# Kernel optimization log

Measured on AMD Instinct MI355X. Metric: run time of the kernel, lower is better.

The kernel has to match this reference:

```python
import jax, jax.numpy as jnp
import numpy as np

D = 1024
H = 4
HD = D // H
B = 256
L = 64
DILATIONS = (1, 4, 8, 16)


def setup_inputs() -> dict:
    key = jax.random.key(0)
    ks = jax.random.split(key, 12)
    s = 1.0 / np.sqrt(D)
    return {
        "x": jax.random.normal(ks[0], (B, D), jnp.float32),
        "hist": jax.random.normal(ks[1], (L, B, D), jnp.float32),
        "Wq": jax.random.normal(ks[2], (D, D), jnp.float32) * s,
        "bq": jnp.zeros((D,), jnp.float32),
        "Wk": jax.random.normal(ks[3], (D, D), jnp.float32) * s,
        "bk": jnp.zeros((D,), jnp.float32),
        "Wv": jax.random.normal(ks[4], (D, D), jnp.float32) * s,
        "bv": jnp.zeros((D,), jnp.float32),
        "Wo": jax.random.normal(ks[5], (D, D), jnp.float32) * s,
        "bo": jnp.zeros((D,), jnp.float32),
        "dil_w": jnp.full((len(DILATIONS),), 1.0 / len(DILATIONS), jnp.float32),
        "gamma": jnp.ones((D,), jnp.float32),
        "beta": jnp.zeros((D,), jnp.float32),
    }


def reference(x, hist, Wq, bq, Wk, bk, Wv, bv, Wo, bo, dil_w, gamma, beta):
    scale = 1.0 / np.sqrt(HD)
    q = (x @ Wq + bq).reshape(B, H, HD)  # (B, H, HD)
    attended = []
    for d in DILATIONS:
        # history frames at stride d, concatenated along dim 0 (faithful to torch.cat)
        frames = hist[::d].reshape(-1, D)              # (T', D), T' = ceil(L/d)*B
        k = (frames @ Wk + bk).reshape(-1, H, HD)      # (T', H, HD)
        v = (frames @ Wv + bv).reshape(-1, H, HD)
        s = jnp.einsum('bhd,thd->bht', q, k) * scale   # (B, H, T')
        a = jax.nn.softmax(s, axis=-1)
        attended.append(jnp.einsum('bht,thd->bhd', a, v).reshape(B, D))
    w = jax.nn.softmax(dil_w, axis=0)
    combined = sum(w[i] * attended[i] for i in range(len(DILATIONS)))
    y = x + combined @ Wo + bo
    mu = jnp.mean(y, axis=-1, keepdims=True)
    var = jnp.var(y, axis=-1, keepdims=True)
    return (y - mu) / jnp.sqrt(var + 1e-5) * gamma + beta
```

## Files before the change

kernel.cpp:

```cpp
#include <hip/hip_runtime.h>


#define DD    1024
#define TALL  16384

typedef _Float16 half8  __attribute__((ext_vector_type(8)));
typedef _Float16 half4v __attribute__((ext_vector_type(4)));
typedef float    floatx4 __attribute__((ext_vector_type(4)));
typedef unsigned int u32;

static const size_t OFF_WOT  = 0;
static const size_t OFF_WV16 = 2097152;
static const size_t OFF_WK16 = 4194304;
static const size_t OFF_WQ16 = 6291456;
static const size_t OFF_XB   = 8388608;
static const size_t OFF_G    = 8912896;
static const size_t OFF_WVOT = 11010048;
static const size_t OFF_WQKT = 19398656;
static const size_t OFF_BVWO = 27787264;
static const size_t OFF_BQK  = 27791360;
static const size_t OFF_PHR  = 27807744;
static const size_t OFF_OPP  = 29904896;
static const size_t OFF_HB   = 38293504;
static const size_t OFF_HT   = 71848960;
static const size_t OFF_S    = 105403392;

__device__ __forceinline__ size_t chunk16_off(int g) {
  if (g < 4)  return (size_t)g * 2097152;
  if (g < 8)  return 19398656 + (size_t)(g - 4) * 2097152;
  if (g < 12) return 29904896 + (size_t)(g - 8) * 2097152;
  return 38293504 + (size_t)(g - 12) * 2097152;
}

__device__ __forceinline__ int frame_of(int g, int j) {
  if (g < 12) { int m = g * 4 + j; return m + m / 3 + 1; }
  if (g < 14) return 4 + 8 * ((g - 12) * 4 + j);
  if (g == 14) return 8 + 16 * j;
  return 16 * j;
}
__device__ __forceinline__ size_t foff(int g, int t) {
  return (size_t)frame_of(g, t >> 3) * 512 + (size_t)(t & 7) * 64;
}

__device__ __forceinline__ void gl_lds16(const void* g, void* l) {
  __builtin_amdgcn_global_load_lds((const __attribute__((address_space(1))) u32*)g,
                                   (__attribute__((address_space(3))) u32*)l, 16, 0, 0);
}

__global__ void prep_kernel(const float* __restrict__ Wo, const float* __restrict__ Wv,
                            const float* __restrict__ Wk, const float* __restrict__ Wq,
                            const float* __restrict__ x, const float* __restrict__ hist,
                            _Float16* __restrict__ WoT, _Float16* __restrict__ Wv16,
                            _Float16* __restrict__ Wk16, _Float16* __restrict__ Wq16,
                            _Float16* __restrict__ xb, _Float16* __restrict__ histb,
                            _Float16* __restrict__ histT) {
  int bid = blockIdx.x, tid = threadIdx.x;
  if (bid < 1024) {
    int k0 = (bid & 31) * 32, n0 = (bid >> 5) * 32;
    __shared__ float t32[32][33];
    int tx = tid & 31, ty = tid >> 5;
#pragma unroll
    for (int i = 0; i < 4; i++) {
      int r = ty + i * 8;
      t32[r][tx] = Wo[(size_t)(k0 + r) * DD + n0 + tx];
    }
    __syncthreads();
#pragma unroll
    for (int i = 0; i < 4; i++) {
      int r = ty + i * 8;
      WoT[(size_t)(n0 + r) * DD + k0 + tx] = (_Float16)t32[tx][r];
    }
  } else if (bid < 4352) {
    const float* src; _Float16* dst; size_t i;
    if (bid < 2048)      { src = Wv; dst = Wv16; i = (size_t)(bid - 1024) * 256 + tid; }
    else if (bid < 3072) { src = Wk; dst = Wk16; i = (size_t)(bid - 2048) * 256 + tid; }
    else if (bid < 4096) { src = Wq; dst = Wq16; i = (size_t)(bid - 3072) * 256 + tid; }
    else                 { src = x;  dst = xb;   i = (size_t)(bid - 4096) * 256 + tid; }
    float4 v = ((const float4*)src)[i];
    half4v h = {(_Float16)v.x, (_Float16)v.y, (_Float16)v.z, (_Float16)v.w};
    *(half4v*)(dst + 4 * i) = h;
  } else {
    int tb = bid - 4352;
    int t0 = (tb & 255) * 64, f0 = (tb >> 8) * 64;
    __shared__ _Float16 lt[64][72];
    int r = tid >> 2, c0 = (tid & 3) * 16;
    half8 s0, s1;
#pragma unroll
    for (int i = 0; i < 4; i++) {
      float4 v = *(const float4*)&hist[(size_t)(t0 + r) * 1024 + f0 + c0 + i * 4];
      half4v h = {(_Float16)v.x, (_Float16)v.y, (_Float16)v.z, (_Float16)v.w};
      *(half4v*)&lt[r][c0 + i * 4] = h;
      if (i < 2) { s0[i*4]=h[0]; s0[i*4+1]=h[1]; s0[i*4+2]=h[2]; s0[i*4+3]=h[3]; }
      else { s1[(i-2)*4]=h[0]; s1[(i-2)*4+1]=h[1]; s1[(i-2)*4+2]=h[2]; s1[(i-2)*4+3]=h[3]; }
    }
    *(half8*)&histb[(size_t)(t0 + r) * 1024 + f0 + c0] = s0;
    *(half8*)&histb[(size_t)(t0 + r) * 1024 + f0 + c0 + 8] = s1;
    __syncthreads();
    int fr = tid >> 2, tc0 = (tid & 3) * 16;
    half8 o0, o1;
#pragma unroll
    for (int j = 0; j < 8; j++) { o0[j] = lt[tc0 + j][fr]; o1[j] = lt[tc0 + 8 + j][fr]; }
    *(half8*)&histT[(size_t)(f0 + fr) * TALL + t0 + tc0] = o0;
    *(half8*)&histT[(size_t)(f0 + fr) * TALL + t0 + tc0 + 8] = o1;
  }
}

__device__ __forceinline__ void gemm_core(const _Float16* __restrict__ A, size_t lda,
                                          const _Float16* __restrict__ B, size_t ldb,
                                          int kIters, _Float16* As, _Float16* Bs,
                                          int tid, floatx4 acc[4][4]) {
  int lane = tid & 63, w = tid >> 6;
  int l15 = lane & 15, quad = lane >> 4;
  int wm = (w >> 1) * 64, wn = (w & 1) * 64;
  int swz = ((tid & 3) ^ ((tid >> 3) & 3)) * 8;
  int pch = (quad ^ ((l15 >> 1) & 3)) * 8;
  const char* gA0 = (const char*)(A + (size_t)(tid >> 2) * lda + swz);
  const char* gA1 = (const char*)(A + ((size_t)(tid >> 2) + 64) * lda + swz);
  const char* gB0 = (const char*)(B + (size_t)(tid >> 2) * ldb + swz);
  const char* gB1 = (const char*)(B + ((size_t)(tid >> 2) + 64) * ldb + swz);
  _Float16* lA = As + w * 512;
  _Float16* lB = Bs + w * 512;
#define GC_STAGE(buf, k)                                    \
  do {                                                      \
    size_t off_ = (size_t)(k) * 64;                         \
    gl_lds16(gA0 + off_, lA + (buf) * 4096);                \
    gl_lds16(gA1 + off_, lA + (buf) * 4096 + 2048);         \
    gl_lds16(gB0 + off_, lB + (buf) * 4096);                \
    gl_lds16(gB1 + off_, lB + (buf) * 4096 + 2048);         \
  } while (0)
#define GC_STEP(buf, k)                                                       \
  do {                                                                        \
    if ((k) + 1 < kIters) asm volatile("s_waitcnt vmcnt(4)" ::: "memory");    \
    else                  asm volatile("s_waitcnt vmcnt(0)" ::: "memory");    \
    asm volatile("s_barrier" ::: "memory");                                   \
    const _Float16* Ac_ = As + (buf) * 4096;                                  \
    const _Float16* Bc_ = Bs + (buf) * 4096;                                  \
    half8 a_[4];                                                              \
    _Pragma("unroll")                                                         \
    for (int mi = 0; mi < 4; mi++)                                            \
      a_[mi] = *(const half8*)&Ac_[(wm + mi * 16 + l15) * 32 + pch];          \
    _Pragma("unroll")                                                         \
    for (int ni = 0; ni < 4; ni++) {                                          \
      half8 b8_ = *(const half8*)&Bc_[(wn + ni * 16 + l15) * 32 + pch];       \
      _Pragma("unroll")                                                       \
      for (int mi = 0; mi < 4; mi++)                                          \
        acc[mi][ni] = __builtin_amdgcn_mfma_f32_16x16x32_f16(a_[mi], b8_,     \
                                                             acc[mi][ni], 0, 0, 0); \
    }                                                                         \
    asm volatile("s_waitcnt lgkmcnt(0)" ::: "memory");                        \
    asm volatile("s_barrier" ::: "memory");                                   \
    if ((k) + 2 < kIters) GC_STAGE(buf, (k) + 2);                             \
  } while (0)
  GC_STAGE(0, 0);
  GC_STAGE(1, 1);
  for (int kk = 0; kk < kIters; kk += 2) {
    GC_STEP(0, kk);
    GC_STEP(1, kk + 1);
  }
#undef GC_STEP
#undef GC_STAGE
}

template <typename OFF>
__device__ __forceinline__ void gemm256_run(const _Float16* __restrict__ A, size_t lda,
                                            const _Float16* __restrict__ B, size_t ldb,
                                            OFF off, _Float16* As, _Float16* Bs,
                                            int tid, floatx4 acc[8][4]) {
  int lane = tid & 63, w = tid >> 6;
  int l15 = lane & 15, quad = lane >> 4;
  int wr = w >> 2, wc = w & 3;
  int pch = (quad ^ ((l15 >> 1) & 3)) * 8;
  int srow = tid >> 2;
  int schunk = (tid & 3) ^ ((tid >> 3) & 3);
  const char* gA0 = (const char*)(A + (size_t)srow * lda + schunk * 8);
  const char* gA1 = (const char*)(A + (size_t)(srow + 128) * lda + schunk * 8);
  const char* gB0 = (const char*)(B + (size_t)srow * ldb + schunk * 8);
  const char* gB1 = (const char*)(B + (size_t)(srow + 128) * ldb + schunk * 8);
  _Float16* lA = As + w * 512;
  _Float16* lB = Bs + w * 512;
#define PSTA(buf, t)                                          \
  do { size_t o_ = off(t);                                    \
    gl_lds16(gA0 + o_, lA + (buf) * 8192);                    \
    gl_lds16(gA1 + o_, lA + (buf) * 8192 + 4096);             \
  } while (0)
#define PSTB(buf, t)                                          \
  do { size_t o_ = off(t);                                    \
    gl_lds16(gB0 + o_, lB + (buf) * 8192);                    \
    gl_lds16(gB1 + o_, lB + (buf) * 8192 + 4096);             \
  } while (0)
  PSTA(0, 0); PSTB(0, 0);
  PSTA(1, 1); PSTB(1, 1);
  PSTA(2, 2); PSTB(2, 2);
  for (int t = 0; t < 32; ++t) {
    int buf = t & 3;
    if (t + 2 < 32)      asm volatile("s_waitcnt vmcnt(8)" ::: "memory");
    else if (t + 1 < 32) asm volatile("s_waitcnt vmcnt(4)" ::: "memory");
    else                 asm volatile("s_waitcnt vmcnt(0)" ::: "memory");
    asm volatile("s_barrier" ::: "memory");
    const _Float16* Ac = As + buf * 8192;
    const _Float16* Bc = Bs + buf * 8192;
    half8 b8[4], a8[4];
#pragma unroll
    for (int ni = 0; ni < 4; ni++)
      b8[ni] = *(const half8*)&Bc[(wc * 64 + ni * 16 + l15) * 32 + pch];
#pragma unroll
    for (int mi = 0; mi < 4; mi++)
      a8[mi] = *(const half8*)&Ac[(wr * 128 + mi * 16 + l15) * 32 + pch];
    if (t + 3 < 32) PSTA((t + 3) & 3, t + 3);
    asm volatile("s_waitcnt lgkmcnt(0)" ::: "memory");
    __builtin_amdgcn_s_setprio(1);
#pragma unroll
    for (int mi = 0; mi < 4; mi++)
#pragma unroll
      for (int ni = 0; ni < 4; ni++)
        acc[mi][ni] = __builtin_amdgcn_mfma_f32_16x16x32_f16(a8[mi], b8[ni], acc[mi][ni], 0, 0, 0);
    __builtin_amdgcn_s_setprio(0);
#pragma unroll
    for (int mi = 0; mi < 4; mi++)
      a8[mi] = *(const half8*)&Ac[(wr * 128 + 64 + mi * 16 + l15) * 32 + pch];
    if (t + 3 < 32) PSTB((t + 3) & 3, t + 3);
    asm volatile("s_waitcnt lgkmcnt(0)" ::: "memory");
    __builtin_amdgcn_s_setprio(1);
#pragma unroll
    for (int mi = 0; mi < 4; mi++)
#pragma unroll
      for (int ni = 0; ni < 4; ni++)
        acc[4 + mi][ni] = __builtin_amdgcn_mfma_f32_16x16x32_f16(a8[mi], b8[ni], acc[4 + mi][ni], 0, 0, 0);
    __builtin_amdgcn_s_setprio(0);
  }
#undef PSTA
#undef PSTB
}

struct LinOff { __device__ __forceinline__ size_t operator()(int t) const { return (size_t)t * 64; } };
struct ClsOff { int g; __device__ __forceinline__ size_t operator()(int t) const { return foff(g, t); } };

template <bool OUTF32>
__launch_bounds__(256, 3)
__global__ void gemm_f16_kernel(const _Float16* __restrict__ A, size_t lda, size_t aoffz,
                                const _Float16* __restrict__ B, size_t ldb, size_t boffz,
                                int kIters, const float* __restrict__ bias, size_t biasoffz,
                                float scale, void* __restrict__ C, size_t ldc, size_t coffz) {
  __shared__ __align__(16) _Float16 As[8192];
  __shared__ __align__(16) _Float16 Bs[8192];
  int tid = threadIdx.x;
  const _Float16* Ab = A + aoffz * blockIdx.z + (size_t)(blockIdx.y * 128) * lda;
  const _Float16* Bb = B + boffz * blockIdx.z + (size_t)(blockIdx.x * 128) * ldb;
  floatx4 acc[4][4];
  floatx4 zero = {0.f, 0.f, 0.f, 0.f};
#pragma unroll
  for (int a = 0; a < 4; a++)
#pragma unroll
    for (int b = 0; b < 4; b++) acc[a][b] = zero;
  gemm_core(Ab, lda, Bb, ldb, kIters, As, Bs, tid, acc);
  int lane = tid & 63, w = tid >> 6;
  int l15 = lane & 15, quad = lane >> 4;
  int wm = (w >> 1) * 64, wn = (w & 1) * 64;
#pragma unroll
  for (int mi = 0; mi < 4; mi++)
#pragma unroll
    for (int ni = 0; ni < 4; ni++) {
      int colg = blockIdx.x * 128 + wn + ni * 16 + l15;
      float bv = bias ? bias[biasoffz * blockIdx.z + colg] : 0.f;
#pragma unroll
      for (int r = 0; r < 4; r++) {
        int rowg = blockIdx.y * 128 + wm + mi * 16 + quad * 4 + r;
        float v = (acc[mi][ni][r] + bv) * scale;
        size_t idx = coffz * blockIdx.z + (size_t)rowg * ldc + colg;
        if (OUTF32) ((float*)C)[idx] = v;
        else ((_Float16*)C)[idx] = (_Float16)v;
      }
    }
}

__launch_bounds__(256, 3)
__global__ void gemm_g_kernel(const _Float16* __restrict__ xb, const _Float16* __restrict__ WQKT,
                              float* __restrict__ gpart) {
  __shared__ __align__(16) _Float16 As[8192];
  __shared__ __align__(16) _Float16 Bs[8192];
  int tid = threadIdx.x;
  int z = blockIdx.z, sp = z >> 2, h = z & 3;
  const _Float16* Ab = xb + sp * 256 + (size_t)(blockIdx.y * 128) * 1024;
  const _Float16* Bb = WQKT + (size_t)h * 1048576 + sp * 256 + (size_t)(blockIdx.x * 128) * 1024;
  floatx4 acc[4][4];
  floatx4 zero = {0.f, 0.f, 0.f, 0.f};
#pragma unroll
  for (int a = 0; a < 4; a++)
#pragma unroll
    for (int b = 0; b < 4; b++) acc[a][b] = zero;
  gemm_core(Ab, 1024, Bb, 1024, 8, As, Bs, tid, acc);
  int lane = tid & 63, w = tid >> 6;
  int l15 = lane & 15, quad = lane >> 4;
  int wm = (w >> 1) * 64, wn = (w & 1) * 64;
#pragma unroll
  for (int mi = 0; mi < 4; mi++)
#pragma unroll
    for (int ni = 0; ni < 4; ni++) {
      int col = blockIdx.x * 128 + wn + ni * 16 + l15;
#pragma unroll
      for (int r = 0; r < 4; r++) {
        int row = blockIdx.y * 128 + wm + mi * 16 + quad * 4 + r;
        gpart[(size_t)z * 262144 + (size_t)row * 1024 + col] = acc[mi][ni][r];
      }
    }
}

__global__ void reduce_g_kernel(const float* __restrict__ gpart, const float* __restrict__ bqk,
                                _Float16* __restrict__ G) {
  size_t e4 = ((size_t)blockIdx.x * 256 + threadIdx.x) * 4;
  int h = (int)(e4 >> 18);
  size_t rem = e4 & 262143;
  int d = (int)(e4 & 1023);
  float4 s = *(const float4*)&bqk[h * 1024 + d];
#pragma unroll
  for (int sp = 0; sp < 4; sp++) {
    float4 p = *(const float4*)&gpart[(size_t)(sp * 4 + h) * 262144 + rem];
    s.x += p.x; s.y += p.y; s.z += p.z; s.w += p.w;
  }
  half4v o = {(_Float16)s.x, (_Float16)s.y, (_Float16)s.z, (_Float16)s.w};
  *(half4v*)&G[e4] = o;
}

__launch_bounds__(256, 3)
__global__ void wpack_kernel(const _Float16* __restrict__ WoT, const _Float16* __restrict__ Wv16,
                             const _Float16* __restrict__ Wk16, const _Float16* __restrict__ Wq16,
                             const float* __restrict__ bv, const float* __restrict__ bq,
                             _Float16* __restrict__ WVOT, _Float16* __restrict__ WQKT,
                             float* __restrict__ bvwo, float* __restrict__ bqk) {
  __shared__ __align__(16) _Float16 As[8192];
  __shared__ __align__(16) _Float16 Bs[8192];
  int bid = blockIdx.x, tid = threadIdx.x;
  if (bid < 512) {
    bool isQK = bid >= 256;
    int g = bid & 255;
    int x = g & 7, y = (g >> 3) & 7, z = g >> 6;
    const _Float16* A = isQK ? Wk16 : WoT;
    const _Float16* B = isQK ? Wq16 : Wv16;
    const _Float16* Ab = A + 256 * z + (size_t)(y * 128) * 1024;
    const _Float16* Bb = B + 256 * z + (size_t)(x * 128) * 1024;
    floatx4 acc[4][4];
    floatx4 zero = {0.f, 0.f, 0.f, 0.f};
#pragma unroll
    for (int a = 0; a < 4; a++)
#pragma unroll
      for (int b = 0; b < 4; b++) acc[a][b] = zero;
    gemm_core(Ab, 1024, Bb, 1024, 8, As, Bs, tid, acc);
    float scale = isQK ? 0.0625f : 1.0f;
    _Float16* C = isQK ? WQKT : WVOT;
    size_t ldc = isQK ? 1024 : 4096;
    size_t zoff = isQK ? (size_t)1048576 * z : (size_t)1024 * z;
    int lane = tid & 63, w = tid >> 6;
    int l15 = lane & 15, quad = lane >> 4;
    int wm = (w >> 1) * 64, wn = (w & 1) * 64;
#pragma unroll
    for (int mi = 0; mi < 4; mi++)
#pragma unroll
      for (int ni = 0; ni < 4; ni++) {
        int col = x * 128 + wn + ni * 16 + l15;
#pragma unroll
        for (int r = 0; r < 4; r++) {
          int row = y * 128 + wm + mi * 16 + quad * 4 + r;
          C[zoff + (size_t)row * ldc + col] = (_Float16)(acc[mi][ni][r] * scale);
        }
      }
  } else if (bid < 516) {
    int j = (bid - 512) * 256 + tid;
    const half8* row = (const half8*)(WoT + (size_t)j * 1024);
    float a = 0.f;
    for (int c = 0; c < 128; c++) {
      half8 w8 = row[c];
#pragma unroll
      for (int e = 0; e < 8; e++) a += bv[c * 8 + e] * (float)w8[e];
    }
    bvwo[j] = a;
  } else {
    int idx = (bid - 516) * 256 + tid;
    int h = idx >> 10, f = idx & 1023;
    const _Float16* row = Wk16 + (size_t)f * 1024 + h * 256;
    float a = 0.f;
    for (int n = 0; n < 256; n++) a += bq[h * 256 + n] * (float)row[n];
    bqk[idx] = a * 0.0625f;
  }
}

__launch_bounds__(512, 2)
__global__ void gemm256_s_kernel(const _Float16* __restrict__ G, const _Float16* __restrict__ histb,
                                 _Float16* __restrict__ Eout, float* __restrict__ zframe) {
  __shared__ __align__(16) _Float16 SM[65536];
  _Float16* As = SM;
  _Float16* Bs = SM + 32768;
  int bid = blockIdx.x, tid = threadIdx.x;
  int h = bid >> 6, nt = bid & 63;
  const _Float16* Ab = G + (size_t)h * 262144;
  const _Float16* Bb = histb + (size_t)(nt * 256) * 1024;
  floatx4 acc[8][4];
  floatx4 zero = {0.f, 0.f, 0.f, 0.f};
#pragma unroll
  for (int a = 0; a < 8; a++)
#pragma unroll
    for (int b = 0; b < 4; b++) acc[a][b] = zero;
  gemm256_run(Ab, 1024, Bb, 1024, LinOff{}, As, Bs, tid, acc);
  int lane = tid & 63, w = tid >> 6;
  int l15 = lane & 15, quad = lane >> 4;
  int wr = w >> 2, wc = w & 3;
  __syncthreads();
#pragma unroll
  for (int mh = 0; mh < 2; mh++)
#pragma unroll
    for (int mi = 0; mi < 4; mi++)
#pragma unroll
      for (int ni = 0; ni < 4; ni++) {
        int col = wc * 64 + ni * 16 + l15;
#pragma unroll
        for (int r = 0; r < 4; r++) {
          int row = wr * 128 + mh * 64 + mi * 16 + quad * 4 + r;
          int colsw = col ^ (((row >> 2) & 3) << 3);
          SM[row * 256 + colsw] = (_Float16)__expf(acc[mh * 4 + mi][ni][r]);
        }
      }
  __syncthreads();
  int c32 = lane & 31, hs = lane >> 5;
#pragma unroll
  for (int it = 0; it < 16; it++) {
    int row = w * 32 + it * 2 + hs;
    int cs = (c32 * 8) ^ (((row >> 2) & 3) << 3);
    half8 v = *(const half8*)&SM[row * 256 + cs];
    float s = 0.f;
#pragma unroll
    for (int j = 0; j < 8; j++) s += (float)v[j];
#pragma unroll
    for (int off = 1; off <= 16; off <<= 1) s += __shfl_xor(s, off, 64);
    *(half8*)&Eout[(size_t)h * 4194304 + (size_t)row * TALL + nt * 256 + c32 * 8] = v;
    if (c32 == 0) zframe[(size_t)(h * 256 + row) * 64 + nt] = s;
  }
}

__launch_bounds__(512, 2)
__global__ void gemm256_ph_kernel(const _Float16* __restrict__ E, const _Float16* __restrict__ histT,
                                  const float* __restrict__ zframe, const float* __restrict__ dil_w,
                                  float* __restrict__ w4, char* __restrict__ ws) {
  __shared__ __align__(16) _Float16 SM[65536];
  int bid = blockIdx.x, tid = threadIdx.x;
  if (bid == 256) {
    float w0 = dil_w[0], w1 = dil_w[1], w2 = dil_w[2], w3 = dil_w[3];
    float wmx = fmaxf(fmaxf(w0, w1), fmaxf(w2, w3));
    float e0 = __expf(w0 - wmx), e1 = __expf(w1 - wmx), e2 = __expf(w2 - wmx), e3 = __expf(w3 - wmx);
    float wsum = e0 + e1 + e2 + e3;
#pragma unroll
    for (int i = 0; i < 2; i++) {
      int row = i * 512 + tid;
      const float* z = zframe + (size_t)row * 64;
      float z1 = 0.f, z4 = 0.f, z8 = 0.f, z16 = 0.f;
#pragma unroll
      for (int f = 0; f < 64; f++) {
        float v = z[f];
        z1 += v;
        if (!(f & 3))  z4 += v;
        if (!(f & 7))  z8 += v;
        if (!(f & 15)) z16 += v;
      }
      float b0 = (e0 / wsum) / z1 * 256.0f;
      float b1 = (e1 / wsum) / z4 * 256.0f;
      float b2 = (e2 / wsum) / z8 * 256.0f;
      float b3 = (e3 / wsum) / z16 * 256.0f;
      float* wr = w4 + (size_t)row * 4;
      wr[0] = b0;
      wr[1] = b0 + b1;
      wr[2] = b0 + b1 + b2;
      wr[3] = b0 + b1 + b2 + b3;
    }
    return;
  }
  _Float16* As = SM;
  _Float16* Bs = SM + 32768;
  int xcd = bid & 7, slot = bid >> 3;
  int g = xcd + 8 * (slot >> 4);
  int member = slot & 15;
  int h = member >> 2, nt = member & 3;
  const _Float16* A = E + (size_t)h * 4194304;
  const _Float16* B = histT + (size_t)(nt * 256) * TALL;
  floatx4 acc[8][4];
  floatx4 zero = {0.f, 0.f, 0.f, 0.f};
#pragma unroll
  for (int a = 0; a < 8; a++)
#pragma unroll
    for (int b = 0; b < 4; b++) acc[a][b] = zero;
  gemm256_run(A, TALL, B, TALL, ClsOff{g}, As, Bs, tid, acc);
  int lane = tid & 63, w = tid >> 6;
  int l15 = lane & 15, quad = lane >> 4;
  int wr = w >> 2, wc = w & 3;
  __syncthreads();
#pragma unroll
  for (int mh = 0; mh < 2; mh++)
#pragma unroll
    for (int mi = 0; mi < 4; mi++)
#pragma unroll
      for (int ni = 0; ni < 4; ni++) {
        int col = wc * 64 + ni * 16 + l15;
#pragma unroll
        for (int r = 0; r < 4; r++) {
          int row = wr * 128 + mh * 64 + mi * 16 + quad * 4 + r;
          int colsw = col ^ (((row >> 2) & 3) << 3);
          SM[row * 256 + colsw] = (_Float16)acc[mh * 4 + mi][ni][r];
        }
      }
  __syncthreads();
  _Float16* chunk = (_Float16*)(ws + chunk16_off(g));
  int c32 = lane & 31, hs = lane >> 5;
  int colbase = h * 1024 + nt * 256;
#pragma unroll
  for (int it = 0; it < 16; it++) {
    int row = w * 32 + it * 2 + hs;
    int cs = (c32 * 8) ^ (((row >> 2) & 3) << 3);
    half8 v = *(const half8*)&SM[row * 256 + cs];
    *(half8*)&chunk[(size_t)row * 4096 + colbase + c32 * 8] = v;
  }
}

__global__ void reduce_ph_kernel(const char* __restrict__ ws, const float* __restrict__ w4,
                                 _Float16* __restrict__ PHred) {
  size_t e8 = ((size_t)blockIdx.x * 256 + threadIdx.x) * 8;
  int q = (int)(e8 >> 12);
  int h = (int)((e8 >> 10) & 3);
  const float* wr = w4 + (size_t)(h * 256 + q) * 4;
  float sA[8] = {0,0,0,0,0,0,0,0}, sB[8] = {0,0,0,0,0,0,0,0};
  float sC[8] = {0,0,0,0,0,0,0,0}, sD[8] = {0,0,0,0,0,0,0,0};
#pragma unroll
  for (int g = 0; g < 12; g++) {
    const _Float16* p = (const _Float16*)(ws + chunk16_off(g));
    half8 v = *(const half8*)&p[e8];
#pragma unroll
    for (int j = 0; j < 8; j++) sA[j] += (float)v[j];
  }
#pragma unroll
  for (int g = 12; g < 14; g++) {
    const _Float16* p = (const _Float16*)(ws + chunk16_off(g));
    half8 v = *(const half8*)&p[e8];
#pragma unroll
    for (int j = 0; j < 8; j++) sB[j] += (float)v[j];
  }
  {
    const _Float16* p = (const _Float16*)(ws + chunk16_off(14));
    half8 v = *(const half8*)&p[e8];
#pragma unroll
    for (int j = 0; j < 8; j++) sC[j] += (float)v[j];
  }
  {
    const _Float16* p = (const _Float16*)(ws + chunk16_off(15));
    half8 v = *(const half8*)&p[e8];
#pragma unroll
    for (int j = 0; j < 8; j++) sD[j] += (float)v[j];
  }
  float wA = wr[0], wB = wr[1], wC = wr[2], wD = wr[3];
  half8 o;
#pragma unroll
  for (int j = 0; j < 8; j++)
    o[j] = (_Float16)(wA * sA[j] + wB * sB[j] + wC * sC[j] + wD * sD[j]);
  *(half8*)&PHred[e8] = o;
}

__global__ void ln_kernel(const float* __restrict__ x, const float* __restrict__ part2,
                          const float* __restrict__ bo, const float* __restrict__ bvwo,
                          const float* __restrict__ gamma, const float* __restrict__ beta,
                          float* __restrict__ out) {
  int b = blockIdx.x, t = threadIdx.x;
  __shared__ float red[8];
  float y[4];
  float sum = 0.f, sq = 0.f;
#pragma unroll
  for (int i = 0; i < 4; i++) {
    int j = t + i * 256;
    float v = x[(size_t)b * 1024 + j] + bo[j] + bvwo[j];
#pragma unroll
    for (int z = 0; z < 16; z++) v += part2[(size_t)z * 262144 + (size_t)b * 1024 + j];
    y[i] = v;
    sum += v;
    sq += v * v;
  }
#pragma unroll
  for (int off = 1; off < 64; off <<= 1) {
    sum += __shfl_xor(sum, off, 64);
    sq += __shfl_xor(sq, off, 64);
  }
  int w = t >> 6, lane = t & 63;
  if (lane == 0) { red[w] = sum; red[4 + w] = sq; }
  __syncthreads();
  sum = red[0] + red[1] + red[2] + red[3];
  sq = red[4] + red[5] + red[6] + red[7];
  float mu = sum * (1.f / 1024.f);
  float var = sq * (1.f / 1024.f) - mu * mu;
  float inv = rsqrtf(var + 1e-5f);
#pragma unroll
  for (int i = 0; i < 4; i++) {
    int j = t + i * 256;
    out[(size_t)b * 1024 + j] = (y[i] - mu) * inv * gamma[j] + beta[j];
  }
}

extern "C" void kernel_launch(void* const* d_in, const int* in_sizes, int n_in,
                              void* d_out, int out_size, void* d_ws, size_t ws_size,
                              hipStream_t stream) {
  const float* x     = (const float*)d_in[0];
  const float* hist  = (const float*)d_in[1];
  const float* Wq    = (const float*)d_in[2];
  const float* bq    = (const float*)d_in[3];
  const float* Wk    = (const float*)d_in[4];
  const float* Wv    = (const float*)d_in[6];
  const float* bv    = (const float*)d_in[7];
  const float* Wo    = (const float*)d_in[8];
  const float* bo    = (const float*)d_in[9];
  const float* dil_w = (const float*)d_in[10];
  const float* gamma = (const float*)d_in[11];
  const float* beta  = (const float*)d_in[12];
  char* ws = (char*)d_ws;

  _Float16* WoT   = (_Float16*)(ws + OFF_WOT);
  _Float16* Wv16  = (_Float16*)(ws + OFF_WV16);
  _Float16* Wk16  = (_Float16*)(ws + OFF_WK16);
  _Float16* Wq16  = (_Float16*)(ws + OFF_WQ16);
  _Float16* xb    = (_Float16*)(ws + OFF_XB);
  _Float16* G     = (_Float16*)(ws + OFF_G);
  _Float16* WVOT  = (_Float16*)(ws + OFF_WVOT);
  _Float16* WQKT  = (_Float16*)(ws + OFF_WQKT);
  float* bvwo     = (float*)(ws + OFF_BVWO);
  float* bqk      = (float*)(ws + OFF_BQK);
  _Float16* PHred = (_Float16*)(ws + OFF_PHR);
  float* oppart   = (float*)(ws + OFF_OPP);
  _Float16* histb = (_Float16*)(ws + OFF_HB);
  _Float16* histT = (_Float16*)(ws + OFF_HT);
  _Float16* Eb    = (_Float16*)(ws + OFF_S);
  float* gpart    = (float*)(ws + OFF_S);
  float* zframe   = (float*)(ws + OFF_PHR);
  float* w4       = (float*)(ws + OFF_G);

  prep_kernel<<<dim3(8448), 256, 0, stream>>>(Wo, Wv, Wk, Wq, x, hist,
                                              WoT, Wv16, Wk16, Wq16, xb, histb, histT);
  wpack_kernel<<<dim3(532), 256, 0, stream>>>(WoT, Wv16, Wk16, Wq16, bv, bq,
                                              WVOT, WQKT, bvwo, bqk);
  gemm_g_kernel<<<dim3(8, 2, 16), 256, 0, stream>>>(xb, WQKT, gpart);
  reduce_g_kernel<<<dim3(1024), 256, 0, stream>>>(gpart, bqk, G);
  gemm256_s_kernel<<<dim3(256), 512, 0, stream>>>(G, histb, Eb, zframe);
  gemm256_ph_kernel<<<dim3(257), 512, 0, stream>>>(Eb, histT, zframe, dil_w, w4, ws);
  reduce_ph_kernel<<<dim3(512), 256, 0, stream>>>(ws, w4, PHred);
  gemm_f16_kernel<true><<<dim3(8, 2, 16), 256, 0, stream>>>(
      PHred, 4096, 256, WVOT, 4096, 256, 8, nullptr, 0, 1.0f / 256.0f,
      (void*)oppart, 1024, 262144);
  ln_kernel<<<dim3(256), 256, 0, stream>>>(x, oppart, bo, bvwo, gamma, beta, (float*)d_out);
}
```

Measured before the change: 300.7 us.

## Retile P·hist GEMM to 256x128 tiles with 256 threads and inline double-buffered loop

The second attention GEMM now uses 256x128 output tiles with 256-thread blocks, launching 512 tiles plus one weight block instead of 256 larger 512-thread blocks. The shared gemm256_run helper is replaced by an inline loop that double-buffers global-to-LDS copies with explicit vmcnt waits, barriers and MFMA priority raising. The aim is better CU occupancy and wave count, and smaller LDS per block so more blocks fit on a CU. In exchange each tile reuses its A rows across fewer columns, so the E matrix is read twice as often.

```diff
diff --git a/kernel.cpp b/kernel.cpp
--- a/kernel.cpp
+++ b/kernel.cpp
@@ -435,20 +435,20 @@
   }
 }
 
-__launch_bounds__(512, 2)
+__launch_bounds__(256, 2)
 __global__ void gemm256_ph_kernel(const _Float16* __restrict__ E, const _Float16* __restrict__ histT,
                                   const float* __restrict__ zframe, const float* __restrict__ dil_w,
                                   float* __restrict__ w4, char* __restrict__ ws) {
-  __shared__ __align__(16) _Float16 SM[65536];
+  __shared__ __align__(16) _Float16 SM[32768];
   int bid = blockIdx.x, tid = threadIdx.x;
-  if (bid == 256) {
+  if (bid == 512) {
     float w0 = dil_w[0], w1 = dil_w[1], w2 = dil_w[2], w3 = dil_w[3];
     float wmx = fmaxf(fmaxf(w0, w1), fmaxf(w2, w3));
     float e0 = __expf(w0 - wmx), e1 = __expf(w1 - wmx), e2 = __expf(w2 - wmx), e3 = __expf(w3 - wmx);
     float wsum = e0 + e1 + e2 + e3;
 #pragma unroll
-    for (int i = 0; i < 2; i++) {
-      int row = i * 512 + tid;
+    for (int i = 0; i < 4; i++) {
+      int row = i * 256 + tid;
       const float* z = zframe + (size_t)row * 64;
       float z1 = 0.f, z4 = 0.f, z8 = 0.f, z16 = 0.f;
 #pragma unroll
@@ -472,48 +472,93 @@
     return;
   }
   _Float16* As = SM;
-  _Float16* Bs = SM + 32768;
+  _Float16* Bs = SM + 16384;
   int xcd = bid & 7, slot = bid >> 3;
-  int g = xcd + 8 * (slot >> 4);
-  int member = slot & 15;
-  int h = member >> 2, nt = member & 3;
+  int g = xcd + 8 * (slot >> 5);
+  int member = slot & 31;
+  int h = member >> 3, nt = member & 7;
+  int lane = tid & 63, w = tid >> 6;
+  int l15 = lane & 15, quad = lane >> 4;
+  int wr = w >> 1, wc = w & 1;
+  int pch = (quad ^ ((l15 >> 1) & 3)) * 8;
+  int srow = tid >> 2;
+  int schunk = (tid & 3) ^ ((tid >> 3) & 3);
   const _Float16* A = E + (size_t)h * 4194304;
-  const _Float16* B = histT + (size_t)(nt * 256) * TALL;
+  const _Float16* B = histT + (size_t)(nt * 128) * TALL;
+  const char* gA0 = (const char*)(A + (size_t)srow * TALL + schunk * 8);
+  const char* gA1 = (const char*)(A + (size_t)(srow + 64) * TALL + schunk * 8);
+  const char* gA2 = (const char*)(A + (size_t)(srow + 128) * TALL + schunk * 8);
+  const char* gA3 = (const char*)(A + (size_t)(srow + 192) * TALL + schunk * 8);
+  const char* gB0 = (const char*)(B + (size_t)srow * TALL + schunk * 8);
+  const char* gB1 = (const char*)(B + (size_t)(srow + 64) * TALL + schunk * 8);
+  _Float16* lA = As + w * 512;
+  _Float16* lB = Bs + w * 512;
   floatx4 acc[8][4];
   floatx4 zero = {0.f, 0.f, 0.f, 0.f};
 #pragma unroll
   for (int a = 0; a < 8; a++)
 #pragma unroll
     for (int b = 0; b < 4; b++) acc[a][b] = zero;
-  gemm256_run(A, TALL, B, TALL, ClsOff{g}, As, Bs, tid, acc);
-  int lane = tid & 63, w = tid >> 6;
-  int l15 = lane & 15, quad = lane >> 4;
-  int wr = w >> 2, wc = w & 3;
+#define HST(buf, t)                                           \
+  do { size_t o_ = foff(g, t);                                \
+    gl_lds16(gA0 + o_, lA + (buf) * 8192);                    \
+    gl_lds16(gA1 + o_, lA + (buf) * 8192 + 2048);             \
+    gl_lds16(gA2 + o_, lA + (buf) * 8192 + 4096);             \
+    gl_lds16(gA3 + o_, lA + (buf) * 8192 + 6144);             \
+    gl_lds16(gB0 + o_, lB + (buf) * 4096);                    \
+    gl_lds16(gB1 + o_, lB + (buf) * 4096 + 2048);             \
+  } while (0)
+  HST(0, 0);
+  HST(1, 1);
+  for (int t = 0; t < 32; ++t) {
+    int buf = t & 1;
+    if (t + 1 < 32) asm volatile("s_waitcnt vmcnt(6)" ::: "memory");
+    else            asm volatile("s_waitcnt vmcnt(0)" ::: "memory");
+    asm volatile("s_barrier" ::: "memory");
+    const _Float16* Ac = As + buf * 8192;
+    const _Float16* Bc = Bs + buf * 4096;
+    half8 b8[4], a8[8];
+#pragma unroll
+    for (int ni = 0; ni < 4; ni++)
+      b8[ni] = *(const half8*)&Bc[(wc * 64 + ni * 16 + l15) * 32 + pch];
+#pragma unroll
+    for (int mi = 0; mi < 8; mi++)
+      a8[mi] = *(const half8*)&Ac[(wr * 128 + mi * 16 + l15) * 32 + pch];
+    asm volatile("s_waitcnt lgkmcnt(0)" ::: "memory");
+    __builtin_amdgcn_s_setprio(1);
+#pragma unroll
+    for (int mi = 0; mi < 8; mi++)
+#pragma unroll
+      for (int ni = 0; ni < 4; ni++)
+        acc[mi][ni] = __builtin_amdgcn_mfma_f32_16x16x32_f16(a8[mi], b8[ni], acc[mi][ni], 0, 0, 0);
+    __builtin_amdgcn_s_setprio(0);
+    asm volatile("s_barrier" ::: "memory");
+    if (t + 2 < 32) HST(buf, t + 2);
+  }
+#undef HST
   __syncthreads();
 #pragma unroll
-  for (int mh = 0; mh < 2; mh++)
-#pragma unroll
-    for (int mi = 0; mi < 4; mi++)
-#pragma unroll
-      for (int ni = 0; ni < 4; ni++) {
-        int col = wc * 64 + ni * 16 + l15;
-#pragma unroll
-        for (int r = 0; r < 4; r++) {
-          int row = wr * 128 + mh * 64 + mi * 16 + quad * 4 + r;
-          int colsw = col ^ (((row >> 2) & 3) << 3);
-          SM[row * 256 + colsw] = (_Float16)acc[mh * 4 + mi][ni][r];
-        }
+  for (int mi = 0; mi < 8; mi++)
+#pragma unroll
+    for (int ni = 0; ni < 4; ni++) {
+      int col = wc * 64 + ni * 16 + l15;
+#pragma unroll
+      for (int r = 0; r < 4; r++) {
+        int row = wr * 128 + mi * 16 + quad * 4 + r;
+        int colsw = col ^ (((row >> 2) & 3) << 3);
+        SM[row * 128 + colsw] = (_Float16)acc[mi][ni][r];
       }
+    }
   __syncthreads();
   _Float16* chunk = (_Float16*)(ws + chunk16_off(g));
-  int c32 = lane & 31, hs = lane >> 5;
-  int colbase = h * 1024 + nt * 256;
+  int c16 = lane & 15, rq = lane >> 4;
+  int colbase = h * 1024 + nt * 128;
 #pragma unroll
   for (int it = 0; it < 16; it++) {
-    int row = w * 32 + it * 2 + hs;
-    int cs = (c32 * 8) ^ (((row >> 2) & 3) << 3);
-    half8 v = *(const half8*)&SM[row * 256 + cs];
-    *(half8*)&chunk[(size_t)row * 4096 + colbase + c32 * 8] = v;
+    int row = w * 64 + it * 4 + rq;
+    int cs = (c16 * 8) ^ (((row >> 2) & 3) << 3);
+    half8 v = *(const half8*)&SM[row * 128 + cs];
+    *(half8*)&chunk[(size_t)row * 4096 + colbase + c16 * 8] = v;
   }
 }
 
@@ -640,7 +685,7 @@
   gemm_g_kernel<<<dim3(8, 2, 16), 256, 0, stream>>>(xb, WQKT, gpart);
   reduce_g_kernel<<<dim3(1024), 256, 0, stream>>>(gpart, bqk, G);
   gemm256_s_kernel<<<dim3(256), 512, 0, stream>>>(G, histb, Eb, zframe);
-  gemm256_ph_kernel<<<dim3(257), 512, 0, stream>>>(Eb, histT, zframe, dil_w, w4, ws);
+  gemm256_ph_kernel<<<dim3(513), 256, 0, stream>>>(Eb, histT, zframe, dil_w, w4, ws);
   reduce_ph_kernel<<<dim3(512), 256, 0, stream>>>(ws, w4, PHred);
   gemm_f16_kernel<true><<<dim3(8, 2, 16), 256, 0, stream>>>(
       PHred, 4096, 256, WVOT, 4096, 256, 8, nullptr, 0, 1.0f / 256.0f,
```

Result: no change. 298.0 us (-0.9%).
